# Performance work log

Measured on AMD Instinct MI355X. Metric: run time of the kernel, lower is better.

## Reference

```python
import jax, jax.numpy as jnp
import numpy as np


def setup_inputs() -> dict:
    key = jax.random.key(0)
    ks = jax.random.split(key, 5)
    B, P_LEN, D = 16, 1024, 512
    scale = 0.02
    return {
        "P": jax.random.normal(ks[0], (B, P_LEN, D), dtype=jnp.float32),
        "w_atten": jax.random.normal(ks[1], (3 * D,), dtype=jnp.float32) * scale,
        "w1": jax.random.normal(ks[2], (2 * D, D), dtype=jnp.float32) * scale,
        "w2": jax.random.normal(ks[3], (2 * D, D), dtype=jnp.float32) * scale,
        "w3": jax.random.normal(ks[4], (2 * D, D), dtype=jnp.float32) * scale,
        "b1": jnp.zeros((D,), dtype=jnp.float32),
        "b2": jnp.zeros((D,), dtype=jnp.float32),
        "b3": jnp.zeros((D,), dtype=jnp.float32),
    }


def reference(P, w_atten, w1, w2, w3, b1, b2, b3):
    # P: (b, p, d). Original builds a (b, p, 3d, p) concat tensor; the score
    # A[b,i,j] = wa . P_i + wb . P_j + wc . (P_i * P_j) factorizes exactly:
    d = P.shape[-1]
    wa, wb, wc = w_atten[:d], w_atten[d:2 * d], w_atten[2 * d:]
    si = P @ wa                                   # (b, p)  contribution of row token i
    sj = P @ wb                                   # (b, p)  contribution of col token j
    A = si[:, :, None] + sj[:, None, :] + jnp.einsum("bid,bjd->bij", P * wc, P)
    SA = jax.nn.softmax(A, axis=2)                # softmax over j
    attn_res = jnp.einsum("bij,bjd->bid", SA, P)  # (b, p, d)
    # Fuse gate (DecayingDropout is identity at inference)
    Pc = jnp.concatenate([P, attn_res], axis=2)   # (b, p, 2d)
    z = jnp.tanh(Pc @ w1 + b1)
    r = jax.nn.sigmoid(Pc @ w2 + b2)
    f = jax.nn.sigmoid(Pc @ w3 + b3)
    return r * P + f * z
```

## Files before the change

kernel.cpp:

```cpp
#include <hip/hip_runtime.h>
#include <stdint.h>

#define S_LEN 1024
#define DDIM  512
#define NBATCH 16

typedef __attribute__((ext_vector_type(8))) short bf16x8;
typedef __attribute__((ext_vector_type(4))) float f32x4;
typedef unsigned short ushort_t;

__device__ __forceinline__ unsigned short f2bf(float x) {
  union { float f; uint32_t u; } v; v.f = x;
  return (unsigned short)((v.u + 0x7fffu + ((v.u >> 16) & 1u)) >> 16);
}
__device__ __forceinline__ float bf2f(unsigned short h) {
  union { float f; uint32_t u; } v; v.u = ((uint32_t)h) << 16;
  return v.f;
}

#define GL16(g, l) __builtin_amdgcn_global_load_lds(                          \
    (const __attribute__((address_space(1))) void*)(g),                       \
    (__attribute__((address_space(3))) void*)(l), 16, 0, 0)

__global__ __launch_bounds__(256) void prep_rows(
    const float* __restrict__ P, const float* __restrict__ w_atten,
    unsigned short* __restrict__ Pbf, unsigned short* __restrict__ Qbf,
    float* __restrict__ sj) {
  int wave = threadIdx.x >> 6, lane = threadIdx.x & 63;
  int row = blockIdx.x * 4 + wave;
  const float* prow = P + (size_t)row * DDIM;
  float s = 0.f;
#pragma unroll
  for (int h = 0; h < 2; ++h) {
    int d = h * 256 + lane * 4;
    float4 p  = *(const float4*)(prow + d);
    float4 wb = *(const float4*)(w_atten + DDIM + d);
    float4 wc = *(const float4*)(w_atten + 2 * DDIM + d);
    s += p.x * wb.x + p.y * wb.y + p.z * wb.z + p.w * wb.w;
    ushort4 pb, qb;
    pb.x = f2bf(p.x); pb.y = f2bf(p.y); pb.z = f2bf(p.z); pb.w = f2bf(p.w);
    qb.x = f2bf(p.x * wc.x); qb.y = f2bf(p.y * wc.y);
    qb.z = f2bf(p.z * wc.z); qb.w = f2bf(p.w * wc.w);
    *(ushort4*)(Pbf + (size_t)row * DDIM + d) = pb;
    *(ushort4*)(Qbf + (size_t)row * DDIM + d) = qb;
  }
#pragma unroll
  for (int o = 32; o; o >>= 1) s += __shfl_xor(s, o);
  if (lane == 0) sj[row] = s;
}

__global__ __launch_bounds__(256) void transpose_f2b(
    const float* __restrict__ in, unsigned short* __restrict__ out,
    int R, int C, long inStride, long outStride) {
  __shared__ unsigned short T[64][65];
  in  += (size_t)blockIdx.z * inStride;
  out += (size_t)blockIdx.z * outStride;
  int c0 = blockIdx.x * 64, r0 = blockIdx.y * 64;
  int tx = threadIdx.x & 63, ty = threadIdx.x >> 6;
#pragma unroll
  for (int rr = 0; rr < 16; ++rr) {
    int rl = ty * 16 + rr;
    T[rl][tx] = f2bf(in[(size_t)(r0 + rl) * C + c0 + tx]);
  }
  __syncthreads();
#pragma unroll
  for (int rr = 0; rr < 16; ++rr) {
    int cl = ty * 16 + rr;
    out[(size_t)(c0 + cl) * R + r0 + tx] = T[tx][cl];
  }
}

__global__ __launch_bounds__(256) void transpose_b2b(
    const unsigned short* __restrict__ in, unsigned short* __restrict__ out,
    int R, int C, long inStride, long outStride) {
  __shared__ unsigned short T[64][65];
  in  += (size_t)blockIdx.z * inStride;
  out += (size_t)blockIdx.z * outStride;
  int c0 = blockIdx.x * 64, r0 = blockIdx.y * 64;
  int tx = threadIdx.x & 63, ty = threadIdx.x >> 6;
#pragma unroll
  for (int rr = 0; rr < 16; ++rr) {
    int rl = ty * 16 + rr;
    T[rl][tx] = in[(size_t)(r0 + rl) * C + c0 + tx];
  }
  __syncthreads();
#pragma unroll
  for (int rr = 0; rr < 16; ++rr) {
    int cl = ty * 16 + rr;
    out[(size_t)(c0 + cl) * R + r0 + tx] = T[tx][cl];
  }
}

#define GSTEP(KT)                                                             \
  if constexpr ((KT) < NT) {                                                  \
    if constexpr ((KT) + 2 < NT) {                                            \
      ushort_t* dA_ = lA[((KT) + 2) % 3];                                     \
      ushort_t* dB_ = lB[((KT) + 2) % 3];                                     \
      GL16(aLo0 + ((KT) + 2) * 32, dA_ + lbase);                              \
      GL16(aLo1 + ((KT) + 2) * 32, dA_ + 2048 + lbase);                       \
      GL16(bB0 + ((KT) + 2) * 32, dB_ + lbase);                               \
      GL16(bB1 + ((KT) + 2) * 32, dB_ + 2048 + lbase);                        \
    }                                                                         \
    {                                                                         \
      const ushort_t* Ard_ = lA[(KT) % 3];                                    \
      const ushort_t* Brd_ = lB[(KT) % 3];                                    \
      bf16x8 af[4], bfr[4];                                                   \
      _Pragma("unroll") for (int m = 0; m < 4; ++m)                           \
        af[m] = *(const bf16x8*)(Ard_ + (wr * 64 + m * 16 + frow) * 32 + fswz); \
      _Pragma("unroll") for (int n = 0; n < 4; ++n)                           \
        bfr[n] = *(const bf16x8*)(Brd_ + (wc * 64 + n * 16 + frow) * 32 + fswz); \
      __builtin_amdgcn_s_setprio(1);                                          \
      _Pragma("unroll") for (int m = 0; m < 4; ++m)                           \
      _Pragma("unroll") for (int n = 0; n < 4; ++n)                           \
        acc[m][n] = __builtin_amdgcn_mfma_f32_16x16x32_bf16(af[m], bfr[n],    \
                                                            acc[m][n], 0, 0, 0); \
      __builtin_amdgcn_s_setprio(0);                                          \
    }                                                                         \
    if constexpr ((KT) + 1 < NT) {                                            \
      if constexpr ((KT) + 2 < NT)                                            \
        asm volatile("s_waitcnt vmcnt(4) lgkmcnt(0)" ::: "memory");           \
      else                                                                    \
        asm volatile("s_waitcnt vmcnt(0) lgkmcnt(0)" ::: "memory");           \
      __builtin_amdgcn_s_barrier();                                           \
    }                                                                         \
  }

template<int NT, int EPI>
__global__ __launch_bounds__(256) void gemm_tb(
    const ushort_t* __restrict__ A,
    const ushort_t* __restrict__ Bt,
    ushort_t* __restrict__ C,
    const float* __restrict__ bias,
    int N, int K, int lda,
    long sAb, long sBb, long sCb, long sBiasb) {
  __shared__ __align__(16) ushort_t lA[3][4096];
  __shared__ __align__(16) ushort_t lB[3][4096];
  const int t = threadIdx.x, lane = t & 63, wave = t >> 6;

  const int gx = gridDim.x, gy = gridDim.y;
  int hblk = blockIdx.x + gx * (blockIdx.y + gy * blockIdx.z);
  int cpx = (gx * gy * (int)gridDim.z) >> 3;
  int wk = (hblk & 7) * cpx + (hblk >> 3);
  const int bx = wk % gx; int rem = wk / gx;
  const int by = rem % gy;
  const int z  = rem / gy;

  A += (size_t)z * sAb;
  Bt += (size_t)z * sBb;
  C += (size_t)z * sCb;
  if (bias) bias += (size_t)z * sBiasb;
  const int bm = by * 128, bn = bx * 128;

  f32x4 acc[4][4];
#pragma unroll
  for (int m = 0; m < 4; ++m)
#pragma unroll
    for (int n = 0; n < 4; ++n) acc[m][n] = {0.f, 0.f, 0.f, 0.f};

  const int wr = wave >> 1, wc = wave & 1;
  const int frow = lane & 15;
  const int fswz = (((lane >> 4) ^ ((frow >> 1) & 3)) * 8);
  const int srow = t >> 2;
  const int skc = (((t & 3) ^ ((t >> 3) & 3)) * 8);
  const int lbase = (t & 192) * 8;

  const ushort_t* aLo0 = A + (size_t)(bm + srow) * lda + skc;
  const ushort_t* aLo1 = aLo0 + (size_t)64 * lda;
  const ushort_t* bB0  = Bt + (size_t)(bn + srow) * K + skc;
  const ushort_t* bB1  = bB0 + (size_t)64 * K;

  GL16(aLo0,      lA[0] + lbase);   GL16(aLo1,      lA[0] + 2048 + lbase);
  GL16(bB0,       lB[0] + lbase);   GL16(bB1,       lB[0] + 2048 + lbase);
  GL16(aLo0 + 32, lA[1] + lbase);   GL16(aLo1 + 32, lA[1] + 2048 + lbase);
  GL16(bB0 + 32,  lB[1] + lbase);   GL16(bB1 + 32,  lB[1] + 2048 + lbase);
  asm volatile("s_waitcnt vmcnt(4)" ::: "memory");
  __builtin_amdgcn_s_barrier();

  GSTEP(0)  GSTEP(1)  GSTEP(2)  GSTEP(3)  GSTEP(4)  GSTEP(5)  GSTEP(6)  GSTEP(7)
  GSTEP(8)  GSTEP(9)  GSTEP(10) GSTEP(11) GSTEP(12) GSTEP(13) GSTEP(14) GSTEP(15)
  GSTEP(16) GSTEP(17) GSTEP(18) GSTEP(19) GSTEP(20) GSTEP(21) GSTEP(22) GSTEP(23)
  GSTEP(24) GSTEP(25) GSTEP(26) GSTEP(27) GSTEP(28) GSTEP(29) GSTEP(30) GSTEP(31)

#pragma unroll
  for (int m = 0; m < 4; ++m) {
    int row0 = bm + wr * 64 + m * 16 + (lane >> 4) * 4;
#pragma unroll
    for (int n = 0; n < 4; ++n) {
      int col = bn + wc * 64 + n * 16 + frow;
      float bc = (EPI >= 1) ? bias[col] : 0.f;
#pragma unroll
      for (int i = 0; i < 4; ++i) {
        float v = acc[m][n][i];
        if (EPI == 1) v += bc;
        C[(size_t)(row0 + i) * N + col] = f2bf(v);
      }
    }
  }
}

#define MSTEP(KT)                                                             \
  {                                                                           \
    if constexpr ((KT) + 1 < 32) {                                            \
      ushort_t* dB_ = lB[((KT) + 1) & 1];                                     \
      GL16(bS0 + ((KT) + 1) * 32, dB_ + lbase);                               \
      GL16(bS1 + ((KT) + 1) * 32, dB_ + 2048 + lbase);                        \
      GL16(bS2 + ((KT) + 1) * 32, dB_ + 4096 + lbase);                        \
    }                                                                         \
    if constexpr ((KT) + 2 < 32) {                                            \
      ushort_t* dA_ = lA[((KT) + 2) % 3];                                     \
      if constexpr ((KT) + 2 < 16) {                                          \
        GL16(aLo0 + ((KT) + 2) * 32, dA_ + lbase);                            \
        GL16(aLo1 + ((KT) + 2) * 32, dA_ + 2048 + lbase);                     \
      } else {                                                                \
        GL16(aHi0 + ((KT) + 2 - 16) * 32, dA_ + lbase);                       \
        GL16(aHi1 + ((KT) + 2 - 16) * 32, dA_ + 2048 + lbase);                \
      }                                                                       \
    }                                                                         \
    {                                                                         \
      const ushort_t* Ard_ = lA[(KT) % 3];                                    \
      const ushort_t* Brd_ = lB[(KT) & 1];                                    \
      bf16x8 af[4];                                                           \
      _Pragma("unroll") for (int m = 0; m < 4; ++m)                           \
        af[m] = *(const bf16x8*)(Ard_ + (wr * 64 + m * 16 + frow) * 32 + fswz); \
      _Pragma("unroll") for (int s = 0; s < 3; ++s) {                         \
        bf16x8 b0 = *(const bf16x8*)(Brd_ + s * 2048 +                        \
                                     (wc * 32 + frow) * 32 + fswz);           \
        bf16x8 b1v = *(const bf16x8*)(Brd_ + s * 2048 +                       \
                                      (wc * 32 + 16 + frow) * 32 + fswz);     \
        __builtin_amdgcn_s_setprio(1);                                        \
        _Pragma("unroll") for (int m = 0; m < 4; ++m) {                       \
          acc[s][m][0] = __builtin_amdgcn_mfma_f32_16x16x32_bf16(             \
              af[m], b0, acc[s][m][0], 0, 0, 0);                              \
          acc[s][m][1] = __builtin_amdgcn_mfma_f32_16x16x32_bf16(             \
              af[m], b1v, acc[s][m][1], 0, 0, 0);                             \
        }                                                                     \
        __builtin_amdgcn_s_setprio(0);                                        \
      }                                                                       \
    }                                                                         \
    if constexpr ((KT) + 1 < 32) {                                            \
      if constexpr ((KT) + 2 < 32)                                            \
        asm volatile("s_waitcnt vmcnt(2) lgkmcnt(0)" ::: "memory");           \
      else                                                                    \
        asm volatile("s_waitcnt vmcnt(0) lgkmcnt(0)" ::: "memory");           \
      __builtin_amdgcn_s_barrier();                                           \
    }                                                                         \
  }

__global__ __launch_bounds__(256) void mlp_fused(
    const ushort_t* __restrict__ Pbf,
    const ushort_t* __restrict__ attn,
    const ushort_t* __restrict__ Wt,
    const float* __restrict__ P,
    const float* __restrict__ b1,
    const float* __restrict__ b2,
    const float* __restrict__ b3,
    float* __restrict__ out) {
  __shared__ __align__(16) ushort_t lA[3][4096];
  __shared__ __align__(16) ushort_t lB[2][6144];
  const int t = threadIdx.x, lane = t & 63, wave = t >> 6;

  int hblk = blockIdx.x + 8 * blockIdx.y;
  int wk = (hblk & 7) * 128 + (hblk >> 3);
  const int bx = wk & 7;
  const int by = wk >> 3;
  const int bm = by * 128, bn = bx * 64;

  f32x4 acc[3][4][2];
#pragma unroll
  for (int s = 0; s < 3; ++s)
#pragma unroll
    for (int m = 0; m < 4; ++m)
#pragma unroll
      for (int n = 0; n < 2; ++n) acc[s][m][n] = {0.f, 0.f, 0.f, 0.f};

  const int wr = wave >> 1, wc = wave & 1;
  const int frow = lane & 15;
  const int fswz = (((lane >> 4) ^ ((frow >> 1) & 3)) * 8);
  const int srow = t >> 2;
  const int skc = (((t & 3) ^ ((t >> 3) & 3)) * 8);
  const int lbase = (t & 192) * 8;

  const ushort_t* aLo0 = Pbf + (size_t)(bm + srow) * 512 + skc;
  const ushort_t* aLo1 = aLo0 + (size_t)64 * 512;
  const ushort_t* aHi0 = attn + (size_t)(bm + srow) * 512 + skc;
  const ushort_t* aHi1 = aHi0 + (size_t)64 * 512;
  const ushort_t* bS0 = Wt + (size_t)(bn + srow) * 1024 + skc;
  const ushort_t* bS1 = bS0 + (size_t)512 * 1024;
  const ushort_t* bS2 = bS0 + (size_t)1024 * 1024;

  GL16(aLo0,      lA[0] + lbase);  GL16(aLo1,      lA[0] + 2048 + lbase);
  GL16(bS0,       lB[0] + lbase);  GL16(bS1,       lB[0] + 2048 + lbase);
  GL16(bS2,       lB[0] + 4096 + lbase);
  GL16(aLo0 + 32, lA[1] + lbase);  GL16(aLo1 + 32, lA[1] + 2048 + lbase);
  asm volatile("s_waitcnt vmcnt(2)" ::: "memory");
  __builtin_amdgcn_s_barrier();

  MSTEP(0)  MSTEP(1)  MSTEP(2)  MSTEP(3)  MSTEP(4)  MSTEP(5)  MSTEP(6)  MSTEP(7)
  MSTEP(8)  MSTEP(9)  MSTEP(10) MSTEP(11) MSTEP(12) MSTEP(13) MSTEP(14) MSTEP(15)
  MSTEP(16) MSTEP(17) MSTEP(18) MSTEP(19) MSTEP(20) MSTEP(21) MSTEP(22) MSTEP(23)
  MSTEP(24) MSTEP(25) MSTEP(26) MSTEP(27) MSTEP(28) MSTEP(29) MSTEP(30) MSTEP(31)

#pragma unroll
  for (int m = 0; m < 4; ++m) {
    int row0 = bm + wr * 64 + m * 16 + (lane >> 4) * 4;
#pragma unroll
    for (int n = 0; n < 2; ++n) {
      int col = bn + wc * 32 + n * 16 + frow;
      float B1 = b1[col], B2 = b2[col], B3 = b3[col];
#pragma unroll
      for (int i = 0; i < 4; ++i) {
        size_t idx = (size_t)(row0 + i) * 512 + col;
        float z = tanhf(acc[0][m][n][i] + B1);
        float r = 1.f / (1.f + __expf(-(acc[1][m][n][i] + B2)));
        float f = 1.f / (1.f + __expf(-(acc[2][m][n][i] + B3)));
        out[idx] = r * P[idx] + f * z;
      }
    }
  }
}

__global__ __launch_bounds__(256) void softmax_rows(unsigned short* __restrict__ Sb) {
  __shared__ float red[8];
  unsigned short* p = Sb + (size_t)blockIdx.x * S_LEN;
  int t = threadIdx.x, wave = t >> 6, lane = t & 63;
  ushort4 u = *(ushort4*)(p + t * 4);
  float v0 = bf2f(u.x), v1 = bf2f(u.y), v2 = bf2f(u.z), v3 = bf2f(u.w);
  float mx = fmaxf(fmaxf(v0, v1), fmaxf(v2, v3));
#pragma unroll
  for (int o = 32; o; o >>= 1) mx = fmaxf(mx, __shfl_xor(mx, o));
  if (lane == 0) red[wave] = mx;
  __syncthreads();
  mx = fmaxf(fmaxf(red[0], red[1]), fmaxf(red[2], red[3]));
  float e0 = __expf(v0 - mx), e1 = __expf(v1 - mx);
  float e2 = __expf(v2 - mx), e3 = __expf(v3 - mx);
  float ss = e0 + e1 + e2 + e3;
#pragma unroll
  for (int o = 32; o; o >>= 1) ss += __shfl_xor(ss, o);
  if (lane == 0) red[4 + wave] = ss;
  __syncthreads();
  float inv = 1.f / (red[4] + red[5] + red[6] + red[7]);
  u.x = f2bf(e0 * inv); u.y = f2bf(e1 * inv);
  u.z = f2bf(e2 * inv); u.w = f2bf(e3 * inv);
  *(ushort4*)(p + t * 4) = u;
}

extern "C" void kernel_launch(void* const* d_in, const int* in_sizes, int n_in,
                              void* d_out, int out_size, void* d_ws, size_t ws_size,
                              hipStream_t stream) {
  const float* P  = (const float*)d_in[0];
  const float* wa = (const float*)d_in[1];
  const float* w1 = (const float*)d_in[2];
  const float* w2 = (const float*)d_in[3];
  const float* w3 = (const float*)d_in[4];
  const float* b1 = (const float*)d_in[5];
  const float* b2 = (const float*)d_in[6];
  const float* b3 = (const float*)d_in[7];
  float* out = (float*)d_out;
  char* ws = (char*)d_ws;
  const size_t MB = 1024 * 1024;

  unsigned short* Pbf  = (unsigned short*)(ws + 0);
  unsigned short* PT   = (unsigned short*)(ws + 16 * MB);
  unsigned short* Qbf  = (unsigned short*)(ws + 32 * MB);
  unsigned short* Sbuf = (unsigned short*)(ws + 48 * MB);
  unsigned short* attn = (unsigned short*)(ws + 80 * MB);
  unsigned short* Wt   = (unsigned short*)(ws + 96 * MB);
  float*          sj   = (float*)(ws + 99 * MB);

  const long SD = (long)S_LEN * DDIM;
  const long SS = (long)S_LEN * S_LEN;

  prep_rows<<<4096, 256, 0, stream>>>(P, wa, Pbf, Qbf, sj);
  transpose_b2b<<<dim3(8, 16, NBATCH), 256, 0, stream>>>(Pbf, PT, S_LEN, DDIM, SD, SD);
  transpose_f2b<<<dim3(8, 16, 1), 256, 0, stream>>>(w1, Wt,          1024, 512, 0, 0);
  transpose_f2b<<<dim3(8, 16, 1), 256, 0, stream>>>(w2, Wt + SD,     1024, 512, 0, 0);
  transpose_f2b<<<dim3(8, 16, 1), 256, 0, stream>>>(w3, Wt + 2 * SD, 1024, 512, 0, 0);

  gemm_tb<16, 1><<<dim3(8, 8, NBATCH), 256, 0, stream>>>(
      Qbf, Pbf, Sbuf, sj, 1024, 512, 512, SD, SD, SS, S_LEN);
  softmax_rows<<<16384, 256, 0, stream>>>(Sbuf);
  gemm_tb<32, 0><<<dim3(4, 8, NBATCH), 256, 0, stream>>>(
      Sbuf, PT, attn, nullptr, 512, 1024, 1024, SS, SD, SD, 0);
  mlp_fused<<<dim3(8, 128), 256, 0, stream>>>(
      Pbf, attn, Wt, P, b1, b2, b3, out);
}
```

Measured before the change: 182.7 us.

## Fuse prep and P transpose, batch weight transposes, triple-buffer MLP B tiles

The row-prep kernel now works on 64x64 tiles and writes the transposed bf16 P directly from shared memory, which removes the separate bf16-to-bf16 transpose pass. The wb dot product is emitted as 8 partial sums per row that the score GEMM epilogue adds together. The three weight transposes are merged into one launch. The fused MLP kernel moves from double to triple buffering with a deeper prefetch of the weight tiles and adds an occupancy hint. In exchange it uses more LDS and adds extra partial-sum reads in the GEMM epilogue.

```diff
diff --git a/kernel.cpp b/kernel.cpp
--- a/kernel.cpp
+++ b/kernel.cpp
@@ -22,72 +22,80 @@
     (const __attribute__((address_space(1))) void*)(g),                       \
     (__attribute__((address_space(3))) void*)(l), 16, 0, 0)
 
-__global__ __launch_bounds__(256) void prep_rows(
+__global__ __launch_bounds__(256) void prep_t(
     const float* __restrict__ P, const float* __restrict__ w_atten,
     unsigned short* __restrict__ Pbf, unsigned short* __restrict__ Qbf,
-    float* __restrict__ sj) {
-  int wave = threadIdx.x >> 6, lane = threadIdx.x & 63;
-  int row = blockIdx.x * 4 + wave;
-  const float* prow = P + (size_t)row * DDIM;
+    unsigned short* __restrict__ PT, float* __restrict__ sjpart) {
+  __shared__ unsigned short T[64][66];
+  const int t = threadIdx.x;
+  const int ct = blockIdx.x;
+  const int rs = blockIdx.y;
+  const int rl = t >> 2;
+  const int cq = (t & 3) << 4;
+  const int row = rs * 64 + rl;
+  const int c0 = ct * 64;
+
+  const float* src = P + (size_t)row * DDIM + c0 + cq;
+  const float* wbp = w_atten + DDIM + c0 + cq;
+  const float* wcp = w_atten + 2 * DDIM + c0 + cq;
   float s = 0.f;
-#pragma unroll
-  for (int h = 0; h < 2; ++h) {
-    int d = h * 256 + lane * 4;
-    float4 p  = *(const float4*)(prow + d);
-    float4 wb = *(const float4*)(w_atten + DDIM + d);
-    float4 wc = *(const float4*)(w_atten + 2 * DDIM + d);
+  unsigned short pb[16];
+#pragma unroll
+  for (int q = 0; q < 4; ++q) {
+    float4 p  = ((const float4*)src)[q];
+    float4 wb = ((const float4*)wbp)[q];
+    float4 wc = ((const float4*)wcp)[q];
     s += p.x * wb.x + p.y * wb.y + p.z * wb.z + p.w * wb.w;
-    ushort4 pb, qb;
-    pb.x = f2bf(p.x); pb.y = f2bf(p.y); pb.z = f2bf(p.z); pb.w = f2bf(p.w);
+    pb[q * 4 + 0] = f2bf(p.x); pb[q * 4 + 1] = f2bf(p.y);
+    pb[q * 4 + 2] = f2bf(p.z); pb[q * 4 + 3] = f2bf(p.w);
+    ushort4 qb;
     qb.x = f2bf(p.x * wc.x); qb.y = f2bf(p.y * wc.y);
     qb.z = f2bf(p.z * wc.z); qb.w = f2bf(p.w * wc.w);
-    *(ushort4*)(Pbf + (size_t)row * DDIM + d) = pb;
-    *(ushort4*)(Qbf + (size_t)row * DDIM + d) = qb;
-  }
-#pragma unroll
-  for (int o = 32; o; o >>= 1) s += __shfl_xor(s, o);
-  if (lane == 0) sj[row] = s;
-}
-
-__global__ __launch_bounds__(256) void transpose_f2b(
-    const float* __restrict__ in, unsigned short* __restrict__ out,
-    int R, int C, long inStride, long outStride) {
+    *(ushort4*)(Qbf + (size_t)row * DDIM + c0 + cq + q * 4) = qb;
+  }
+#pragma unroll
+  for (int q = 0; q < 4; ++q) {
+    ushort4 u; u.x = pb[q*4]; u.y = pb[q*4+1]; u.z = pb[q*4+2]; u.w = pb[q*4+3];
+    *(ushort4*)(Pbf + (size_t)row * DDIM + c0 + cq + q * 4) = u;
+  }
+#pragma unroll
+  for (int q = 0; q < 8; ++q) {
+    ushort2 u2; u2.x = pb[q * 2]; u2.y = pb[q * 2 + 1];
+    *(ushort2*)(&T[rl][cq + q * 2]) = u2;
+  }
+  s += __shfl_xor(s, 1);
+  s += __shfl_xor(s, 2);
+  if ((t & 3) == 0) sjpart[(size_t)row * 8 + ct] = s;
+  __syncthreads();
+  const int tx = t & 63, ty = t >> 6;
+  const int b = rs >> 4;
+  const int seq0 = (rs & 15) * 64;
+  unsigned short* ptb = PT + (size_t)b * (DDIM * S_LEN);
+#pragma unroll
+  for (int rr = 0; rr < 16; ++rr) {
+    int cl = ty * 16 + rr;
+    ptb[(size_t)(c0 + cl) * S_LEN + seq0 + tx] = T[tx][cl];
+  }
+}
+
+__global__ __launch_bounds__(256) void transpose_w3(
+    const float* __restrict__ w1, const float* __restrict__ w2,
+    const float* __restrict__ w3, unsigned short* __restrict__ out) {
   __shared__ unsigned short T[64][65];
-  in  += (size_t)blockIdx.z * inStride;
-  out += (size_t)blockIdx.z * outStride;
+  const float* in = (blockIdx.z == 0) ? w1 : ((blockIdx.z == 1) ? w2 : w3);
+  out += (size_t)blockIdx.z * (DDIM * S_LEN);
   int c0 = blockIdx.x * 64, r0 = blockIdx.y * 64;
   int tx = threadIdx.x & 63, ty = threadIdx.x >> 6;
 #pragma unroll
   for (int rr = 0; rr < 16; ++rr) {
     int rl = ty * 16 + rr;
-    T[rl][tx] = f2bf(in[(size_t)(r0 + rl) * C + c0 + tx]);
+    T[rl][tx] = f2bf(in[(size_t)(r0 + rl) * 512 + c0 + tx]);
   }
   __syncthreads();
 #pragma unroll
   for (int rr = 0; rr < 16; ++rr) {
     int cl = ty * 16 + rr;
-    out[(size_t)(c0 + cl) * R + r0 + tx] = T[tx][cl];
-  }
-}
-
-__global__ __launch_bounds__(256) void transpose_b2b(
-    const unsigned short* __restrict__ in, unsigned short* __restrict__ out,
-    int R, int C, long inStride, long outStride) {
-  __shared__ unsigned short T[64][65];
-  in  += (size_t)blockIdx.z * inStride;
-  out += (size_t)blockIdx.z * outStride;
-  int c0 = blockIdx.x * 64, r0 = blockIdx.y * 64;
-  int tx = threadIdx.x & 63, ty = threadIdx.x >> 6;
-#pragma unroll
-  for (int rr = 0; rr < 16; ++rr) {
-    int rl = ty * 16 + rr;
-    T[rl][tx] = in[(size_t)(r0 + rl) * C + c0 + tx];
-  }
-  __syncthreads();
-#pragma unroll
-  for (int rr = 0; rr < 16; ++rr) {
-    int cl = ty * 16 + rr;
-    out[(size_t)(c0 + cl) * R + r0 + tx] = T[tx][cl];
+    out[(size_t)(c0 + cl) * 1024 + r0 + tx] = T[tx][cl];
   }
 }
 
@@ -187,11 +195,15 @@
 #pragma unroll
     for (int n = 0; n < 4; ++n) {
       int col = bn + wc * 64 + n * 16 + frow;
-      float bc = (EPI >= 1) ? bias[col] : 0.f;
+      float bc = 0.f;
+      if (EPI == 2) {
+        const float* q = bias + (size_t)col * 8;
+        bc = ((q[0] + q[1]) + (q[2] + q[3])) + ((q[4] + q[5]) + (q[6] + q[7]));
+      }
 #pragma unroll
       for (int i = 0; i < 4; ++i) {
         float v = acc[m][n][i];
-        if (EPI == 1) v += bc;
+        if (EPI == 2) v += bc;
         C[(size_t)(row0 + i) * N + col] = f2bf(v);
       }
     }
@@ -200,14 +212,9 @@
 
 #define MSTEP(KT)                                                             \
   {                                                                           \
-    if constexpr ((KT) + 1 < 32) {                                            \
-      ushort_t* dB_ = lB[((KT) + 1) & 1];                                     \
-      GL16(bS0 + ((KT) + 1) * 32, dB_ + lbase);                               \
-      GL16(bS1 + ((KT) + 1) * 32, dB_ + 2048 + lbase);                        \
-      GL16(bS2 + ((KT) + 1) * 32, dB_ + 4096 + lbase);                        \
-    }                                                                         \
     if constexpr ((KT) + 2 < 32) {                                            \
       ushort_t* dA_ = lA[((KT) + 2) % 3];                                     \
+      ushort_t* dB_ = lB[((KT) + 2) % 3];                                     \
       if constexpr ((KT) + 2 < 16) {                                          \
         GL16(aLo0 + ((KT) + 2) * 32, dA_ + lbase);                            \
         GL16(aLo1 + ((KT) + 2) * 32, dA_ + 2048 + lbase);                     \
@@ -215,10 +222,13 @@
         GL16(aHi0 + ((KT) + 2 - 16) * 32, dA_ + lbase);                       \
         GL16(aHi1 + ((KT) + 2 - 16) * 32, dA_ + 2048 + lbase);                \
       }                                                                       \
+      GL16(bS0 + ((KT) + 2) * 32, dB_ + lbase);                               \
+      GL16(bS1 + ((KT) + 2) * 32, dB_ + 2048 + lbase);                        \
+      GL16(bS2 + ((KT) + 2) * 32, dB_ + 4096 + lbase);                        \
     }                                                                         \
     {                                                                         \
       const ushort_t* Ard_ = lA[(KT) % 3];                                    \
-      const ushort_t* Brd_ = lB[(KT) & 1];                                    \
+      const ushort_t* Brd_ = lB[(KT) % 3];                                    \
       bf16x8 af[4];                                                           \
       _Pragma("unroll") for (int m = 0; m < 4; ++m)                           \
         af[m] = *(const bf16x8*)(Ard_ + (wr * 64 + m * 16 + frow) * 32 + fswz); \
@@ -239,14 +249,14 @@
     }                                                                         \
     if constexpr ((KT) + 1 < 32) {                                            \
       if constexpr ((KT) + 2 < 32)                                            \
-        asm volatile("s_waitcnt vmcnt(2) lgkmcnt(0)" ::: "memory");           \
+        asm volatile("s_waitcnt vmcnt(5) lgkmcnt(0)" ::: "memory");           \
       else                                                                    \
         asm volatile("s_waitcnt vmcnt(0) lgkmcnt(0)" ::: "memory");           \
       __builtin_amdgcn_s_barrier();                                           \
     }                                                                         \
   }
 
-__global__ __launch_bounds__(256) void mlp_fused(
+__global__ __launch_bounds__(256, 2) void mlp_fused(
     const ushort_t* __restrict__ Pbf,
     const ushort_t* __restrict__ attn,
     const ushort_t* __restrict__ Wt,
@@ -256,7 +266,7 @@
     const float* __restrict__ b3,
     float* __restrict__ out) {
   __shared__ __align__(16) ushort_t lA[3][4096];
-  __shared__ __align__(16) ushort_t lB[2][6144];
+  __shared__ __align__(16) ushort_t lB[3][3 * 2048];
   const int t = threadIdx.x, lane = t & 63, wave = t >> 6;
 
   int hblk = blockIdx.x + 8 * blockIdx.y;
@@ -292,7 +302,9 @@
   GL16(bS0,       lB[0] + lbase);  GL16(bS1,       lB[0] + 2048 + lbase);
   GL16(bS2,       lB[0] + 4096 + lbase);
   GL16(aLo0 + 32, lA[1] + lbase);  GL16(aLo1 + 32, lA[1] + 2048 + lbase);
-  asm volatile("s_waitcnt vmcnt(2)" ::: "memory");
+  GL16(bS0 + 32,  lB[1] + lbase);  GL16(bS1 + 32,  lB[1] + 2048 + lbase);
+  GL16(bS2 + 32,  lB[1] + 4096 + lbase);
+  asm volatile("s_waitcnt vmcnt(5)" ::: "memory");
   __builtin_amdgcn_s_barrier();
 
   MSTEP(0)  MSTEP(1)  MSTEP(2)  MSTEP(3)  MSTEP(4)  MSTEP(5)  MSTEP(6)  MSTEP(7)
@@ -359,25 +371,22 @@
   char* ws = (char*)d_ws;
   const size_t MB = 1024 * 1024;
 
-  unsigned short* Pbf  = (unsigned short*)(ws + 0);
-  unsigned short* PT   = (unsigned short*)(ws + 16 * MB);
-  unsigned short* Qbf  = (unsigned short*)(ws + 32 * MB);
-  unsigned short* Sbuf = (unsigned short*)(ws + 48 * MB);
-  unsigned short* attn = (unsigned short*)(ws + 80 * MB);
-  unsigned short* Wt   = (unsigned short*)(ws + 96 * MB);
-  float*          sj   = (float*)(ws + 99 * MB);
+  unsigned short* Pbf    = (unsigned short*)(ws + 0);
+  unsigned short* PT     = (unsigned short*)(ws + 16 * MB);
+  unsigned short* Qbf    = (unsigned short*)(ws + 32 * MB);
+  unsigned short* Sbuf   = (unsigned short*)(ws + 48 * MB);
+  unsigned short* attn   = (unsigned short*)(ws + 80 * MB);
+  unsigned short* Wt     = (unsigned short*)(ws + 96 * MB);
+  float*          sjpart = (float*)(ws + 99 * MB);
 
   const long SD = (long)S_LEN * DDIM;
   const long SS = (long)S_LEN * S_LEN;
 
-  prep_rows<<<4096, 256, 0, stream>>>(P, wa, Pbf, Qbf, sj);
-  transpose_b2b<<<dim3(8, 16, NBATCH), 256, 0, stream>>>(Pbf, PT, S_LEN, DDIM, SD, SD);
-  transpose_f2b<<<dim3(8, 16, 1), 256, 0, stream>>>(w1, Wt,          1024, 512, 0, 0);
-  transpose_f2b<<<dim3(8, 16, 1), 256, 0, stream>>>(w2, Wt + SD,     1024, 512, 0, 0);
-  transpose_f2b<<<dim3(8, 16, 1), 256, 0, stream>>>(w3, Wt + 2 * SD, 1024, 512, 0, 0);
-
-  gemm_tb<16, 1><<<dim3(8, 8, NBATCH), 256, 0, stream>>>(
-      Qbf, Pbf, Sbuf, sj, 1024, 512, 512, SD, SD, SS, S_LEN);
+  prep_t<<<dim3(8, 256), 256, 0, stream>>>(P, wa, Pbf, Qbf, PT, sjpart);
+  transpose_w3<<<dim3(8, 16, 3), 256, 0, stream>>>(w1, w2, w3, Wt);
+
+  gemm_tb<16, 2><<<dim3(8, 8, NBATCH), 256, 0, stream>>>(
+      Qbf, Pbf, Sbuf, sjpart, 1024, 512, 512, SD, SD, SS, 8 * S_LEN);
   softmax_rows<<<16384, 256, 0, stream>>>(Sbuf);
   gemm_tb<32, 0><<<dim3(4, 8, NBATCH), 256, 0, stream>>>(
       Sbuf, PT, attn, nullptr, 512, 1024, 1024, SS, SD, SD, 0);
```

Measured after the change: 191.4 us. 4.7% more time.

## Triple-buffer MLP weight tiles and merge weight transposes into one launch

Applied to the files above, without the earlier changes.

In the fused MLP gate kernel, the B (weight) tiles move from double to triple buffering. They are now prefetched two K-steps ahead like the A tiles, and the wait counts are adjusted to match. The three separate weight-transpose launches become a single launch with a z dimension of 3, and the MLP kernel gets a launch bound asking for two blocks per CU. The deeper prefetch should hide more load latency but uses more LDS (72KB per block), which may cap occupancy below the requested two blocks.

```diff
diff --git a/kernel.cpp b/kernel.cpp
--- a/kernel.cpp
+++ b/kernel.cpp
@@ -49,27 +49,6 @@
   if (lane == 0) sj[row] = s;
 }
 
-__global__ __launch_bounds__(256) void transpose_f2b(
-    const float* __restrict__ in, unsigned short* __restrict__ out,
-    int R, int C, long inStride, long outStride) {
-  __shared__ unsigned short T[64][65];
-  in  += (size_t)blockIdx.z * inStride;
-  out += (size_t)blockIdx.z * outStride;
-  int c0 = blockIdx.x * 64, r0 = blockIdx.y * 64;
-  int tx = threadIdx.x & 63, ty = threadIdx.x >> 6;
-#pragma unroll
-  for (int rr = 0; rr < 16; ++rr) {
-    int rl = ty * 16 + rr;
-    T[rl][tx] = f2bf(in[(size_t)(r0 + rl) * C + c0 + tx]);
-  }
-  __syncthreads();
-#pragma unroll
-  for (int rr = 0; rr < 16; ++rr) {
-    int cl = ty * 16 + rr;
-    out[(size_t)(c0 + cl) * R + r0 + tx] = T[tx][cl];
-  }
-}
-
 __global__ __launch_bounds__(256) void transpose_b2b(
     const unsigned short* __restrict__ in, unsigned short* __restrict__ out,
     int R, int C, long inStride, long outStride) {
@@ -88,6 +67,27 @@
   for (int rr = 0; rr < 16; ++rr) {
     int cl = ty * 16 + rr;
     out[(size_t)(c0 + cl) * R + r0 + tx] = T[tx][cl];
+  }
+}
+
+__global__ __launch_bounds__(256) void transpose_w3(
+    const float* __restrict__ w1, const float* __restrict__ w2,
+    const float* __restrict__ w3, unsigned short* __restrict__ out) {
+  __shared__ unsigned short T[64][65];
+  const float* in = (blockIdx.z == 0) ? w1 : ((blockIdx.z == 1) ? w2 : w3);
+  out += (size_t)blockIdx.z * (DDIM * S_LEN);
+  int c0 = blockIdx.x * 64, r0 = blockIdx.y * 64;
+  int tx = threadIdx.x & 63, ty = threadIdx.x >> 6;
+#pragma unroll
+  for (int rr = 0; rr < 16; ++rr) {
+    int rl = ty * 16 + rr;
+    T[rl][tx] = f2bf(in[(size_t)(r0 + rl) * 512 + c0 + tx]);
+  }
+  __syncthreads();
+#pragma unroll
+  for (int rr = 0; rr < 16; ++rr) {
+    int cl = ty * 16 + rr;
+    out[(size_t)(c0 + cl) * 1024 + r0 + tx] = T[tx][cl];
   }
 }
 
@@ -200,14 +200,9 @@
 
 #define MSTEP(KT)                                                             \
   {                                                                           \
-    if constexpr ((KT) + 1 < 32) {                                            \
-      ushort_t* dB_ = lB[((KT) + 1) & 1];                                     \
-      GL16(bS0 + ((KT) + 1) * 32, dB_ + lbase);                               \
-      GL16(bS1 + ((KT) + 1) * 32, dB_ + 2048 + lbase);                        \
-      GL16(bS2 + ((KT) + 1) * 32, dB_ + 4096 + lbase);                        \
-    }                                                                         \
     if constexpr ((KT) + 2 < 32) {                                            \
       ushort_t* dA_ = lA[((KT) + 2) % 3];                                     \
+      ushort_t* dB_ = lB[((KT) + 2) % 3];                                     \
       if constexpr ((KT) + 2 < 16) {                                          \
         GL16(aLo0 + ((KT) + 2) * 32, dA_ + lbase);                            \
         GL16(aLo1 + ((KT) + 2) * 32, dA_ + 2048 + lbase);                     \
@@ -215,10 +210,13 @@
         GL16(aHi0 + ((KT) + 2 - 16) * 32, dA_ + lbase);                       \
         GL16(aHi1 + ((KT) + 2 - 16) * 32, dA_ + 2048 + lbase);                \
       }                                                                       \
+      GL16(bS0 + ((KT) + 2) * 32, dB_ + lbase);                               \
+      GL16(bS1 + ((KT) + 2) * 32, dB_ + 2048 + lbase);                        \
+      GL16(bS2 + ((KT) + 2) * 32, dB_ + 4096 + lbase);                        \
     }                                                                         \
     {                                                                         \
       const ushort_t* Ard_ = lA[(KT) % 3];                                    \
-      const ushort_t* Brd_ = lB[(KT) & 1];                                    \
+      const ushort_t* Brd_ = lB[(KT) % 3];                                    \
       bf16x8 af[4];                                                           \
       _Pragma("unroll") for (int m = 0; m < 4; ++m)                           \
         af[m] = *(const bf16x8*)(Ard_ + (wr * 64 + m * 16 + frow) * 32 + fswz); \
@@ -239,14 +237,14 @@
     }                                                                         \
     if constexpr ((KT) + 1 < 32) {                                            \
       if constexpr ((KT) + 2 < 32)                                            \
-        asm volatile("s_waitcnt vmcnt(2) lgkmcnt(0)" ::: "memory");           \
+        asm volatile("s_waitcnt vmcnt(5) lgkmcnt(0)" ::: "memory");           \
       else                                                                    \
         asm volatile("s_waitcnt vmcnt(0) lgkmcnt(0)" ::: "memory");           \
       __builtin_amdgcn_s_barrier();                                           \
     }                                                                         \
   }
 
-__global__ __launch_bounds__(256) void mlp_fused(
+__global__ __launch_bounds__(256, 2) void mlp_fused(
     const ushort_t* __restrict__ Pbf,
     const ushort_t* __restrict__ attn,
     const ushort_t* __restrict__ Wt,
@@ -256,7 +254,7 @@
     const float* __restrict__ b3,
     float* __restrict__ out) {
   __shared__ __align__(16) ushort_t lA[3][4096];
-  __shared__ __align__(16) ushort_t lB[2][6144];
+  __shared__ __align__(16) ushort_t lB[3][3 * 2048];
   const int t = threadIdx.x, lane = t & 63, wave = t >> 6;
 
   int hblk = blockIdx.x + 8 * blockIdx.y;
@@ -292,7 +290,9 @@
   GL16(bS0,       lB[0] + lbase);  GL16(bS1,       lB[0] + 2048 + lbase);
   GL16(bS2,       lB[0] + 4096 + lbase);
   GL16(aLo0 + 32, lA[1] + lbase);  GL16(aLo1 + 32, lA[1] + 2048 + lbase);
-  asm volatile("s_waitcnt vmcnt(2)" ::: "memory");
+  GL16(bS0 + 32,  lB[1] + lbase);  GL16(bS1 + 32,  lB[1] + 2048 + lbase);
+  GL16(bS2 + 32,  lB[1] + 4096 + lbase);
+  asm volatile("s_waitcnt vmcnt(5)" ::: "memory");
   __builtin_amdgcn_s_barrier();
 
   MSTEP(0)  MSTEP(1)  MSTEP(2)  MSTEP(3)  MSTEP(4)  MSTEP(5)  MSTEP(6)  MSTEP(7)
@@ -372,9 +372,7 @@
 
   prep_rows<<<4096, 256, 0, stream>>>(P, wa, Pbf, Qbf, sj);
   transpose_b2b<<<dim3(8, 16, NBATCH), 256, 0, stream>>>(Pbf, PT, S_LEN, DDIM, SD, SD);
-  transpose_f2b<<<dim3(8, 16, 1), 256, 0, stream>>>(w1, Wt,          1024, 512, 0, 0);
-  transpose_f2b<<<dim3(8, 16, 1), 256, 0, stream>>>(w2, Wt + SD,     1024, 512, 0, 0);
-  transpose_f2b<<<dim3(8, 16, 1), 256, 0, stream>>>(w3, Wt + 2 * SD, 1024, 512, 0, 0);
+  transpose_w3<<<dim3(8, 16, 3), 256, 0, stream>>>(w1, w2, w3, Wt);
 
   gemm_tb<16, 1><<<dim3(8, 8, NBATCH), 256, 0, stream>>>(
       Qbf, Pbf, Sbuf, sj, 1024, 512, 512, SD, SD, SS, S_LEN);
```

Result: faster. 173.5 us (median of 2 runs) (-5.0%).
